# Performance work log

Measured on AMD Instinct MI355X. Metric: run time of the kernel, lower is better.

## Reference

```python
import jax, jax.numpy as jnp
import numpy as np

V, C, H, W = 6, 256, 128, 128


def setup_inputs() -> dict:
    key = jax.random.key(0)
    ks = jax.random.split(key, 6)
    return {
        "q": jax.random.normal(ks[0], (V, C, H, W), dtype=jnp.float32),
        "k": jax.random.normal(ks[1], (V, C, H, W), dtype=jnp.float32),
        "v": jax.random.normal(ks[2], (V, C, H, W), dtype=jnp.float32),
        "Wq": jax.random.normal(ks[3], (C, C), dtype=jnp.float32) * (1.0 / np.sqrt(C)),
        "Wk": jax.random.normal(ks[4], (C, C), dtype=jnp.float32) * (1.0 / np.sqrt(C)),
        "Wv": jax.random.normal(ks[5], (C, C), dtype=jnp.float32) * (1.0 / np.sqrt(C)),
    }


def reference(q, k, v, Wq, Wk, Wv):
    # 1x1 conv (no bias) == channel GEMM: [V,C,H,W] x [O,C] -> [V,O,H,W]
    qp = jnp.einsum("vchw,oc->vohw", q, Wq)
    kp = jnp.einsum("vchw,oc->vohw", k, Wk)
    vp = jnp.einsum("vchw,oc->vohw", v, Wv)
    # elementwise q*k, sum over channels (dim=1, keepdim) -> [V,1,H,W]
    att = jnp.sum(qp * kp, axis=1, keepdims=True)
    # softmax over views (dim=0)
    att = jax.nn.softmax(att, axis=0)
    # weight values and sum over views (dim=0, keepdim) -> [1,C,H,W]
    out = jnp.sum(att * vp, axis=0, keepdims=True)
    return out
```

## Files before the change

kernel.cpp:

```cpp
#include <hip/hip_runtime.h>
#include <math.h>

#define HW 16384
#define C_DIM 256
#define V_DIM 6
#define PT 64
#define BK 32
#define KROW 40

typedef short bf16x8 __attribute__((ext_vector_type(8)));
typedef float f32x4 __attribute__((ext_vector_type(4)));

__device__ __forceinline__ void split2(float x, unsigned short& h,
                                       unsigned short& l) {
    unsigned u = __float_as_uint(x);
    h = (unsigned short)(u >> 16);
    float xl = x - __uint_as_float(u & 0xFFFF0000u);
    l = (unsigned short)(__float_as_uint(xl) >> 16);
}

__global__ void compute_M_kernel(const float* __restrict__ Wq,
                                 const float* __restrict__ Wk,
                                 unsigned short* __restrict__ Mh,
                                 unsigned short* __restrict__ Ml) {
    const int i = blockIdx.x;
    const int j = threadIdx.x;
    float a0 = 0.f, a1 = 0.f, a2 = 0.f, a3 = 0.f;
    #pragma unroll 4
    for (int o = 0; o < C_DIM; o += 4) {
        a0 = fmaf(Wq[(o + 0) * C_DIM + i], Wk[(o + 0) * C_DIM + j], a0);
        a1 = fmaf(Wq[(o + 1) * C_DIM + i], Wk[(o + 1) * C_DIM + j], a1);
        a2 = fmaf(Wq[(o + 2) * C_DIM + i], Wk[(o + 2) * C_DIM + j], a2);
        a3 = fmaf(Wq[(o + 3) * C_DIM + i], Wk[(o + 3) * C_DIM + j], a3);
    }
    float acc = (a0 + a1) + (a2 + a3);
    unsigned short h, l;
    split2(acc, h, l);
    Mh[i * C_DIM + j] = h;
    Ml[i * C_DIM + j] = l;
}

__global__ __launch_bounds__(512, 3) void score_kernel(
        const float* __restrict__ q, const float* __restrict__ k,
        const unsigned short* __restrict__ Mh,
        const unsigned short* __restrict__ Ml,
        float* __restrict__ score) {
    const int tid  = threadIdx.x;
    const int lane = tid & 63;
    const int w    = tid >> 6;
    const int pt   = blockIdx.x & 255;
    const int v    = blockIdx.x >> 8;
    const int gp0  = pt * PT;
    const int l15  = lane & 15;
    const int l4   = lane >> 4;

    __shared__ __align__(16) unsigned short Kh_s[2][PT * KROW];
    __shared__ __align__(16) unsigned short Kl_s[2][PT * KROW];
    __shared__ float s_red[8][PT];

    const float* kv = k + (size_t)v * C_DIM * HW + gp0;
    const float* qv = q + (size_t)v * C_DIM * HW + gp0;
    const int ibase = w * 32;

    f32x4 acc[2][4];
    #pragma unroll
    for (int a = 0; a < 2; ++a)
        #pragma unroll
        for (int b = 0; b < 4; ++b)
            acc[a][b] = (f32x4){0.f, 0.f, 0.f, 0.f};

    float kx[3][4];
    bf16x8 Ah[2][2], Al[2][2];
    float qx[32];

    {
        const float* kp = kv + (size_t)(w * 4) * HW + lane;
        float x[4];
        #pragma unroll
        for (int e = 0; e < 4; ++e) x[e] = kp[(size_t)e * HW];
        unsigned short h[4], l[4];
        #pragma unroll
        for (int e = 0; e < 4; ++e) split2(x[e], h[e], l[e]);
        uint2 H, L;
        H.x = (unsigned)h[0] | ((unsigned)h[1] << 16);
        H.y = (unsigned)h[2] | ((unsigned)h[3] << 16);
        L.x = (unsigned)l[0] | ((unsigned)l[1] << 16);
        L.y = (unsigned)l[2] | ((unsigned)l[3] << 16);
        *(uint2*)&Kh_s[0][lane * KROW + w * 4] = H;
        *(uint2*)&Kl_s[0][lane * KROW + w * 4] = L;

        const float* kp1 = kv + (size_t)(1 * BK + w * 4) * HW + lane;
        #pragma unroll
        for (int e = 0; e < 4; ++e) kx[1][e] = kp1[(size_t)e * HW];
        const float* kp2 = kv + (size_t)(2 * BK + w * 4) * HW + lane;
        #pragma unroll
        for (int e = 0; e < 4; ++e) kx[2][e] = kp2[(size_t)e * HW];

        #pragma unroll
        for (int it = 0; it < 2; ++it) {
            int row = ibase + it * 16 + l15;
            Ah[0][it] = *(const bf16x8*)(Mh + (size_t)row * C_DIM + l4 * 8);
            Al[0][it] = *(const bf16x8*)(Ml + (size_t)row * C_DIM + l4 * 8);
        }
    }
    __syncthreads();

    #pragma unroll
    for (int ks = 0; ks < 8; ++ks) {
        const int cur = ks & 1;

        if (ks < 7) {
            #pragma unroll
            for (int it = 0; it < 2; ++it) {
                int row = ibase + it * 16 + l15;
                Ah[cur ^ 1][it] = *(const bf16x8*)(Mh + (size_t)row * C_DIM +
                                                   (ks + 1) * BK + l4 * 8);
                Al[cur ^ 1][it] = *(const bf16x8*)(Ml + (size_t)row * C_DIM +
                                                   (ks + 1) * BK + l4 * 8);
            }
        }
        if (ks < 5) {
            const float* kp = kv + (size_t)((ks + 3) * BK + w * 4) * HW + lane;
            #pragma unroll
            for (int e = 0; e < 4; ++e) kx[ks % 3][e] = kp[(size_t)e * HW];
        }
        if (ks == 7) {
            #pragma unroll
            for (int jt = 0; jt < 4; ++jt)
                #pragma unroll
                for (int it = 0; it < 2; ++it) {
                    int irow = ibase + it * 16 + l4 * 4;
                    const float* qp = qv + (size_t)irow * HW + jt * 16 + l15;
                    #pragma unroll
                    for (int r = 0; r < 4; ++r)
                        qx[jt * 8 + it * 4 + r] = qp[(size_t)r * HW];
                }
        }

        bf16x8 Bh[4];
        #pragma unroll
        for (int jt = 0; jt < 4; ++jt) {
            int bp = jt * 16 + l15;
            Bh[jt] = *(const bf16x8*)&Kh_s[cur][bp * KROW + l4 * 8];
        }
        #pragma unroll
        for (int it = 0; it < 2; ++it)
            #pragma unroll
            for (int jt = 0; jt < 4; ++jt)
                acc[it][jt] = __builtin_amdgcn_mfma_f32_16x16x32_bf16(
                                  Ah[cur][it], Bh[jt], acc[it][jt], 0, 0, 0);
        #pragma unroll
        for (int it = 0; it < 2; ++it)
            #pragma unroll
            for (int jt = 0; jt < 4; ++jt)
                acc[it][jt] = __builtin_amdgcn_mfma_f32_16x16x32_bf16(
                                  Al[cur][it], Bh[jt], acc[it][jt], 0, 0, 0);
        bf16x8 Bl[4];
        #pragma unroll
        for (int jt = 0; jt < 4; ++jt) {
            int bp = jt * 16 + l15;
            Bl[jt] = *(const bf16x8*)&Kl_s[cur][bp * KROW + l4 * 8];
        }
        #pragma unroll
        for (int it = 0; it < 2; ++it)
            #pragma unroll
            for (int jt = 0; jt < 4; ++jt)
                acc[it][jt] = __builtin_amdgcn_mfma_f32_16x16x32_bf16(
                                  Ah[cur][it], Bl[jt], acc[it][jt], 0, 0, 0);

        if (ks < 7) {
            unsigned short h[4], l[4];
            #pragma unroll
            for (int e = 0; e < 4; ++e) split2(kx[(ks + 1) % 3][e], h[e], l[e]);
            uint2 H, L;
            H.x = (unsigned)h[0] | ((unsigned)h[1] << 16);
            H.y = (unsigned)h[2] | ((unsigned)h[3] << 16);
            L.x = (unsigned)l[0] | ((unsigned)l[1] << 16);
            L.y = (unsigned)l[2] | ((unsigned)l[3] << 16);
            *(uint2*)&Kh_s[cur ^ 1][lane * KROW + w * 4] = H;
            *(uint2*)&Kl_s[cur ^ 1][lane * KROW + w * 4] = L;
            __syncthreads();
        }
    }

    float sp[4];
    #pragma unroll
    for (int jt = 0; jt < 4; ++jt) sp[jt] = 0.f;
    #pragma unroll
    for (int jt = 0; jt < 4; ++jt) {
        #pragma unroll
        for (int it = 0; it < 2; ++it)
            #pragma unroll
            for (int r = 0; r < 4; ++r)
                sp[jt] = fmaf(qx[jt * 8 + it * 4 + r], acc[it][jt][r], sp[jt]);
        sp[jt] += __shfl_xor(sp[jt], 16, 64);
        sp[jt] += __shfl_xor(sp[jt], 32, 64);
    }
    if (lane < 16) {
        #pragma unroll
        for (int jt = 0; jt < 4; ++jt)
            s_red[w][jt * 16 + lane] = sp[jt];
    }
    __syncthreads();
    if (tid < PT) {
        float s = 0.f;
        #pragma unroll
        for (int ww = 0; ww < 8; ++ww) s += s_red[ww][tid];
        score[v * HW + gp0 + tid] = s;
    }
}

__global__ void wsplit_kernel(const float* __restrict__ Wv,
                              unsigned short* __restrict__ Wvh,
                              unsigned short* __restrict__ Wvl) {
    const int i = blockIdx.x;
    const int j = threadIdx.x;
    unsigned short h, l;
    split2(Wv[i * C_DIM + j], h, l);
    Wvh[i * C_DIM + j] = h;
    Wvl[i * C_DIM + j] = l;
}

__global__ __launch_bounds__(512, 2) void out_gemm_kernel(
        const float* __restrict__ vin,
        const unsigned short* __restrict__ Wvh,
        const unsigned short* __restrict__ Wvl,
        const float* __restrict__ score,
        float* __restrict__ out) {
    const int tid  = threadIdx.x;
    const int lane = tid & 63;
    const int w    = tid >> 6;
    const int gp0  = blockIdx.x * PT;
    const int l15  = lane & 15;
    const int l4   = lane >> 4;
    const int jg   = w;

    __shared__ __align__(16) unsigned short Xh_s[2][PT * KROW];
    __shared__ __align__(16) unsigned short Xl_s[2][PT * KROW];

    float wr[V_DIM];
    {
        float s[V_DIM];
        float mx = -1e30f;
        #pragma unroll
        for (int vv = 0; vv < V_DIM; ++vv) {
            s[vv] = score[vv * HW + gp0 + lane];
            mx = fmaxf(mx, s[vv]);
        }
        float sum = 0.f;
        #pragma unroll
        for (int vv = 0; vv < V_DIM; ++vv) {
            s[vv] = __expf(s[vv] - mx);
            sum += s[vv];
        }
        float inv = 1.0f / sum;
        #pragma unroll
        for (int vv = 0; vv < V_DIM; ++vv) wr[vv] = s[vv] * inv;
    }

    const float* vbase = vin + gp0 + lane;
    const int obase = w * 32;

    f32x4 acc[2][4];
    #pragma unroll
    for (int a = 0; a < 2; ++a)
        #pragma unroll
        for (int b = 0; b < 4; ++b)
            acc[a][b] = (f32x4){0.f, 0.f, 0.f, 0.f};

    float vx[2][4][V_DIM];
    bf16x8 Ah[2][2], Al[2][2];

    {
        float x0[4][V_DIM];
        #pragma unroll
        for (int vv = 0; vv < V_DIM; ++vv)
            #pragma unroll
            for (int e = 0; e < 4; ++e)
                x0[e][vv] = vbase[(size_t)(vv * C_DIM + jg * 4 + e) * HW];
        unsigned short h[4], l[4];
        #pragma unroll
        for (int e = 0; e < 4; ++e) {
            float s = 0.f;
            #pragma unroll
            for (int vv = 0; vv < V_DIM; ++vv) s = fmaf(wr[vv], x0[e][vv], s);
            split2(s, h[e], l[e]);
        }
        uint2 H, L;
        H.x = (unsigned)h[0] | ((unsigned)h[1] << 16);
        H.y = (unsigned)h[2] | ((unsigned)h[3] << 16);
        L.x = (unsigned)l[0] | ((unsigned)l[1] << 16);
        L.y = (unsigned)l[2] | ((unsigned)l[3] << 16);
        *(uint2*)&Xh_s[0][lane * KROW + jg * 4] = H;
        *(uint2*)&Xl_s[0][lane * KROW + jg * 4] = L;

        #pragma unroll
        for (int vv = 0; vv < V_DIM; ++vv)
            #pragma unroll
            for (int e = 0; e < 4; ++e)
                vx[1][e][vv] = vbase[(size_t)(vv * C_DIM + BK + jg * 4 + e) * HW];

        #pragma unroll
        for (int it = 0; it < 2; ++it) {
            int row = obase + it * 16 + l15;
            Ah[0][it] = *(const bf16x8*)(Wvh + (size_t)row * C_DIM + l4 * 8);
            Al[0][it] = *(const bf16x8*)(Wvl + (size_t)row * C_DIM + l4 * 8);
        }
    }
    __syncthreads();

    #pragma unroll
    for (int ks = 0; ks < 8; ++ks) {
        const int cur = ks & 1;

        if (ks < 7) {
            #pragma unroll
            for (int it = 0; it < 2; ++it) {
                int row = obase + it * 16 + l15;
                Ah[cur ^ 1][it] = *(const bf16x8*)(Wvh + (size_t)row * C_DIM +
                                                   (ks + 1) * BK + l4 * 8);
                Al[cur ^ 1][it] = *(const bf16x8*)(Wvl + (size_t)row * C_DIM +
                                                   (ks + 1) * BK + l4 * 8);
            }
        }
        if (ks < 6) {
            #pragma unroll
            for (int vv = 0; vv < V_DIM; ++vv)
                #pragma unroll
                for (int e = 0; e < 4; ++e)
                    vx[cur][e][vv] = vbase[(size_t)(vv * C_DIM + (ks + 2) * BK +
                                                    jg * 4 + e) * HW];
        }

        bf16x8 Bh[4], Bl[4];
        #pragma unroll
        for (int jt = 0; jt < 4; ++jt) {
            int bp = jt * 16 + l15;
            Bh[jt] = *(const bf16x8*)&Xh_s[cur][bp * KROW + l4 * 8];
            Bl[jt] = *(const bf16x8*)&Xl_s[cur][bp * KROW + l4 * 8];
        }
        #pragma unroll
        for (int it = 0; it < 2; ++it)
            #pragma unroll
            for (int jt = 0; jt < 4; ++jt)
                acc[it][jt] = __builtin_amdgcn_mfma_f32_16x16x32_bf16(
                                  Ah[cur][it], Bh[jt], acc[it][jt], 0, 0, 0);
        #pragma unroll
        for (int it = 0; it < 2; ++it)
            #pragma unroll
            for (int jt = 0; jt < 4; ++jt)
                acc[it][jt] = __builtin_amdgcn_mfma_f32_16x16x32_bf16(
                                  Ah[cur][it], Bl[jt], acc[it][jt], 0, 0, 0);
        #pragma unroll
        for (int it = 0; it < 2; ++it)
            #pragma unroll
            for (int jt = 0; jt < 4; ++jt)
                acc[it][jt] = __builtin_amdgcn_mfma_f32_16x16x32_bf16(
                                  Al[cur][it], Bh[jt], acc[it][jt], 0, 0, 0);

        if (ks < 7) {
            unsigned short h[4], l[4];
            #pragma unroll
            for (int e = 0; e < 4; ++e) {
                float s = 0.f;
                #pragma unroll
                for (int vv = 0; vv < V_DIM; ++vv)
                    s = fmaf(wr[vv], vx[cur ^ 1][e][vv], s);
                split2(s, h[e], l[e]);
            }
            uint2 H, L;
            H.x = (unsigned)h[0] | ((unsigned)h[1] << 16);
            H.y = (unsigned)h[2] | ((unsigned)h[3] << 16);
            L.x = (unsigned)l[0] | ((unsigned)l[1] << 16);
            L.y = (unsigned)l[2] | ((unsigned)l[3] << 16);
            *(uint2*)&Xh_s[cur ^ 1][lane * KROW + jg * 4] = H;
            *(uint2*)&Xl_s[cur ^ 1][lane * KROW + jg * 4] = L;
        }
        __syncthreads();
    }

    #pragma unroll
    for (int it = 0; it < 2; ++it)
        #pragma unroll
        for (int jt = 0; jt < 4; ++jt)
            #pragma unroll
            for (int r = 0; r < 4; ++r) {
                int o = obase + it * 16 + l4 * 4 + r;
                out[(size_t)o * HW + gp0 + jt * 16 + l15] = acc[it][jt][r];
            }
}

extern "C" void kernel_launch(void* const* d_in, const int* in_sizes, int n_in,
                              void* d_out, int out_size, void* d_ws, size_t ws_size,
                              hipStream_t stream) {
    const float* q  = (const float*)d_in[0];
    const float* k  = (const float*)d_in[1];
    const float* v  = (const float*)d_in[2];
    const float* Wq = (const float*)d_in[3];
    const float* Wk = (const float*)d_in[4];
    const float* Wv = (const float*)d_in[5];
    float* out = (float*)d_out;

    unsigned short* Mh = (unsigned short*)d_ws;
    unsigned short* Ml = Mh + C_DIM * C_DIM;
    float* score = (float*)(Ml + C_DIM * C_DIM);

    compute_M_kernel<<<C_DIM, C_DIM, 0, stream>>>(Wq, Wk, Mh, Ml);
    score_kernel<<<V_DIM * 256, 512, 0, stream>>>(q, k, Mh, Ml, score);
    wsplit_kernel<<<C_DIM, C_DIM, 0, stream>>>(Wv, Mh, Ml);
    out_gemm_kernel<<<HW / PT, 512, 0, stream>>>(v, Mh, Ml, score, out);
}
```

Baseline: 121.4 us.

## Stage full K tile in LDS upfront in score kernel, drop per-step double buffering

The score kernel now loads all eight K slabs for its 64-pixel tile at the start, splits them into bf16 hi/lo and stores them in LDS before a single barrier. The main MFMA loop then runs without the per-step global loads, splits and __syncthreads. Q values are loaded directly in the epilogue instead of being prefetched into 32 registers, and the reduction buffer reuses the K LDS space. Launch bounds rise to 4 blocks per CU to try to raise occupancy, at the cost of a larger LDS footprint (about 80KB per block), which may itself limit how many blocks fit, and less overlap of global loads with compute inside a block.

```diff
diff --git a/kernel.cpp b/kernel.cpp
--- a/kernel.cpp
+++ b/kernel.cpp
@@ -7,6 +7,7 @@
 #define PT 64
 #define BK 32
 #define KROW 40
+#define KT (PT * KROW)
 
 typedef short bf16x8 __attribute__((ext_vector_type(8)));
 typedef float f32x4 __attribute__((ext_vector_type(4)));
@@ -40,7 +41,7 @@
     Ml[i * C_DIM + j] = l;
 }
 
-__global__ __launch_bounds__(512, 3) void score_kernel(
+__global__ __launch_bounds__(512, 4) void score_kernel(
         const float* __restrict__ q, const float* __restrict__ k,
         const unsigned short* __restrict__ Mh,
         const unsigned short* __restrict__ Ml,
@@ -54,14 +55,37 @@
     const int l15  = lane & 15;
     const int l4   = lane >> 4;
 
-    __shared__ __align__(16) unsigned short Kh_s[2][PT * KROW];
-    __shared__ __align__(16) unsigned short Kl_s[2][PT * KROW];
-    __shared__ float s_red[8][PT];
+    __shared__ __align__(16) unsigned short Kh_s[8 * KT];
+    __shared__ __align__(16) unsigned short Kl_s[8 * KT];
 
     const float* kv = k + (size_t)v * C_DIM * HW + gp0;
     const float* qv = q + (size_t)v * C_DIM * HW + gp0;
     const int ibase = w * 32;
 
+    {
+        float kx[8][4];
+        #pragma unroll
+        for (int t = 0; t < 8; ++t) {
+            const float* kp = kv + (size_t)(t * BK + w * 4) * HW + lane;
+            #pragma unroll
+            for (int e = 0; e < 4; ++e) kx[t][e] = kp[(size_t)e * HW];
+        }
+        #pragma unroll
+        for (int t = 0; t < 8; ++t) {
+            unsigned short h[4], l[4];
+            #pragma unroll
+            for (int e = 0; e < 4; ++e) split2(kx[t][e], h[e], l[e]);
+            uint2 H, L;
+            H.x = (unsigned)h[0] | ((unsigned)h[1] << 16);
+            H.y = (unsigned)h[2] | ((unsigned)h[3] << 16);
+            L.x = (unsigned)l[0] | ((unsigned)l[1] << 16);
+            L.y = (unsigned)l[2] | ((unsigned)l[3] << 16);
+            *(uint2*)&Kh_s[t * KT + lane * KROW + w * 4] = H;
+            *(uint2*)&Kl_s[t * KT + lane * KROW + w * 4] = L;
+        }
+    }
+    __syncthreads();
+
     f32x4 acc[2][4];
     #pragma unroll
     for (int a = 0; a < 2; ++a)
@@ -69,41 +93,13 @@
         for (int b = 0; b < 4; ++b)
             acc[a][b] = (f32x4){0.f, 0.f, 0.f, 0.f};
 
-    float kx[3][4];
     bf16x8 Ah[2][2], Al[2][2];
-    float qx[32];
-
-    {
-        const float* kp = kv + (size_t)(w * 4) * HW + lane;
-        float x[4];
-        #pragma unroll
-        for (int e = 0; e < 4; ++e) x[e] = kp[(size_t)e * HW];
-        unsigned short h[4], l[4];
-        #pragma unroll
-        for (int e = 0; e < 4; ++e) split2(x[e], h[e], l[e]);
-        uint2 H, L;
-        H.x = (unsigned)h[0] | ((unsigned)h[1] << 16);
-        H.y = (unsigned)h[2] | ((unsigned)h[3] << 16);
-        L.x = (unsigned)l[0] | ((unsigned)l[1] << 16);
-        L.y = (unsigned)l[2] | ((unsigned)l[3] << 16);
-        *(uint2*)&Kh_s[0][lane * KROW + w * 4] = H;
-        *(uint2*)&Kl_s[0][lane * KROW + w * 4] = L;
-
-        const float* kp1 = kv + (size_t)(1 * BK + w * 4) * HW + lane;
-        #pragma unroll
-        for (int e = 0; e < 4; ++e) kx[1][e] = kp1[(size_t)e * HW];
-        const float* kp2 = kv + (size_t)(2 * BK + w * 4) * HW + lane;
-        #pragma unroll
-        for (int e = 0; e < 4; ++e) kx[2][e] = kp2[(size_t)e * HW];
-
-        #pragma unroll
-        for (int it = 0; it < 2; ++it) {
-            int row = ibase + it * 16 + l15;
-            Ah[0][it] = *(const bf16x8*)(Mh + (size_t)row * C_DIM + l4 * 8);
-            Al[0][it] = *(const bf16x8*)(Ml + (size_t)row * C_DIM + l4 * 8);
-        }
-    }
-    __syncthreads();
+    #pragma unroll
+    for (int it = 0; it < 2; ++it) {
+        int row = ibase + it * 16 + l15;
+        Ah[0][it] = *(const bf16x8*)(Mh + (size_t)row * C_DIM + l4 * 8);
+        Al[0][it] = *(const bf16x8*)(Ml + (size_t)row * C_DIM + l4 * 8);
+    }
 
     #pragma unroll
     for (int ks = 0; ks < 8; ++ks) {
@@ -119,29 +115,12 @@
                                                    (ks + 1) * BK + l4 * 8);
             }
         }
-        if (ks < 5) {
-            const float* kp = kv + (size_t)((ks + 3) * BK + w * 4) * HW + lane;
-            #pragma unroll
-            for (int e = 0; e < 4; ++e) kx[ks % 3][e] = kp[(size_t)e * HW];
-        }
-        if (ks == 7) {
-            #pragma unroll
-            for (int jt = 0; jt < 4; ++jt)
-                #pragma unroll
-                for (int it = 0; it < 2; ++it) {
-                    int irow = ibase + it * 16 + l4 * 4;
-                    const float* qp = qv + (size_t)irow * HW + jt * 16 + l15;
-                    #pragma unroll
-                    for (int r = 0; r < 4; ++r)
-                        qx[jt * 8 + it * 4 + r] = qp[(size_t)r * HW];
-                }
-        }
 
         bf16x8 Bh[4];
         #pragma unroll
         for (int jt = 0; jt < 4; ++jt) {
             int bp = jt * 16 + l15;
-            Bh[jt] = *(const bf16x8*)&Kh_s[cur][bp * KROW + l4 * 8];
+            Bh[jt] = *(const bf16x8*)&Kh_s[ks * KT + bp * KROW + l4 * 8];
         }
         #pragma unroll
         for (int it = 0; it < 2; ++it)
@@ -159,7 +138,7 @@
         #pragma unroll
         for (int jt = 0; jt < 4; ++jt) {
             int bp = jt * 16 + l15;
-            Bl[jt] = *(const bf16x8*)&Kl_s[cur][bp * KROW + l4 * 8];
+            Bl[jt] = *(const bf16x8*)&Kl_s[ks * KT + bp * KROW + l4 * 8];
         }
         #pragma unroll
         for (int it = 0; it < 2; ++it)
@@ -167,20 +146,6 @@
             for (int jt = 0; jt < 4; ++jt)
                 acc[it][jt] = __builtin_amdgcn_mfma_f32_16x16x32_bf16(
                                   Ah[cur][it], Bl[jt], acc[it][jt], 0, 0, 0);
-
-        if (ks < 7) {
-            unsigned short h[4], l[4];
-            #pragma unroll
-            for (int e = 0; e < 4; ++e) split2(kx[(ks + 1) % 3][e], h[e], l[e]);
-            uint2 H, L;
-            H.x = (unsigned)h[0] | ((unsigned)h[1] << 16);
-            H.y = (unsigned)h[2] | ((unsigned)h[3] << 16);
-            L.x = (unsigned)l[0] | ((unsigned)l[1] << 16);
-            L.y = (unsigned)l[2] | ((unsigned)l[3] << 16);
-            *(uint2*)&Kh_s[cur ^ 1][lane * KROW + w * 4] = H;
-            *(uint2*)&Kl_s[cur ^ 1][lane * KROW + w * 4] = L;
-            __syncthreads();
-        }
     }
 
     float sp[4];
@@ -189,23 +154,29 @@
     #pragma unroll
     for (int jt = 0; jt < 4; ++jt) {
         #pragma unroll
-        for (int it = 0; it < 2; ++it)
+        for (int it = 0; it < 2; ++it) {
+            int irow = ibase + it * 16 + l4 * 4;
+            const float* qp = qv + (size_t)irow * HW + jt * 16 + l15;
             #pragma unroll
             for (int r = 0; r < 4; ++r)
-                sp[jt] = fmaf(qx[jt * 8 + it * 4 + r], acc[it][jt][r], sp[jt]);
+                sp[jt] = fmaf(qp[(size_t)r * HW], acc[it][jt][r], sp[jt]);
+        }
         sp[jt] += __shfl_xor(sp[jt], 16, 64);
         sp[jt] += __shfl_xor(sp[jt], 32, 64);
     }
+
+    __syncthreads();
+    float* s_red = (float*)Kh_s;
     if (lane < 16) {
         #pragma unroll
         for (int jt = 0; jt < 4; ++jt)
-            s_red[w][jt * 16 + lane] = sp[jt];
+            s_red[w * PT + jt * 16 + lane] = sp[jt];
     }
     __syncthreads();
     if (tid < PT) {
         float s = 0.f;
         #pragma unroll
-        for (int ww = 0; ww < 8; ++ww) s += s_red[ww][tid];
+        for (int ww = 0; ww < 8; ++ww) s += s_red[ww * PT + tid];
         score[v * HW + gp0 + tid] = s;
     }
 }
@@ -235,8 +206,8 @@
     const int l4   = lane >> 4;
     const int jg   = w;
 
-    __shared__ __align__(16) unsigned short Xh_s[2][PT * KROW];
-    __shared__ __align__(16) unsigned short Xl_s[2][PT * KROW];
+    __shared__ __align__(16) unsigned short Xh_s[2][KT];
+    __shared__ __align__(16) unsigned short Xl_s[2][KT];
 
     float wr[V_DIM];
     {
```

Measured after the change: 121.9 us. Within noise of the previous version (+0.4%).

## Make score kernel loop over all views per block with cross-view prefetch

Applied to the files above, without the earlier changes.

The score kernel now launches one block per 64-pixel tile (256 blocks) and loops over the six views inside each block, instead of one block per (view, tile). The K-tile register prefetch runs continuously across view boundaries, with two-deep register buffering replacing three-deep, so the pipeline is not refilled for each view. Q loads are spread over the first four k-steps. Launch bounds drop to 2 waves per SIMD. With only 256 blocks on a chip with 256 CUs, each CU gets a single block, so latency hiding now depends on overlap within the block rather than on several resident blocks per CU.

```diff
diff --git a/kernel.cpp b/kernel.cpp
--- a/kernel.cpp
+++ b/kernel.cpp
@@ -7,6 +7,7 @@
 #define PT 64
 #define BK 32
 #define KROW 40
+#define KT (PT * KROW)
 
 typedef short bf16x8 __attribute__((ext_vector_type(8)));
 typedef float f32x4 __attribute__((ext_vector_type(4)));
@@ -40,7 +41,7 @@
     Ml[i * C_DIM + j] = l;
 }
 
-__global__ __launch_bounds__(512, 3) void score_kernel(
+__global__ __launch_bounds__(512, 2) void score_kernel(
         const float* __restrict__ q, const float* __restrict__ k,
         const unsigned short* __restrict__ Mh,
         const unsigned short* __restrict__ Ml,
@@ -48,18 +49,14 @@
     const int tid  = threadIdx.x;
     const int lane = tid & 63;
     const int w    = tid >> 6;
-    const int pt   = blockIdx.x & 255;
-    const int v    = blockIdx.x >> 8;
-    const int gp0  = pt * PT;
+    const int gp0  = blockIdx.x * PT;
     const int l15  = lane & 15;
     const int l4   = lane >> 4;
 
-    __shared__ __align__(16) unsigned short Kh_s[2][PT * KROW];
-    __shared__ __align__(16) unsigned short Kl_s[2][PT * KROW];
+    __shared__ __align__(16) unsigned short Kh_s[2][KT];
+    __shared__ __align__(16) unsigned short Kl_s[2][KT];
     __shared__ float s_red[8][PT];
 
-    const float* kv = k + (size_t)v * C_DIM * HW + gp0;
-    const float* qv = q + (size_t)v * C_DIM * HW + gp0;
     const int ibase = w * 32;
 
     f32x4 acc[2][4];
@@ -69,12 +66,12 @@
         for (int b = 0; b < 4; ++b)
             acc[a][b] = (f32x4){0.f, 0.f, 0.f, 0.f};
 
-    float kx[3][4];
     bf16x8 Ah[2][2], Al[2][2];
+    float kreg[2][4];
     float qx[32];
 
     {
-        const float* kp = kv + (size_t)(w * 4) * HW + lane;
+        const float* kp = k + gp0 + (size_t)(w * 4) * HW + lane;
         float x[4];
         #pragma unroll
         for (int e = 0; e < 4; ++e) x[e] = kp[(size_t)e * HW];
@@ -89,12 +86,9 @@
         *(uint2*)&Kh_s[0][lane * KROW + w * 4] = H;
         *(uint2*)&Kl_s[0][lane * KROW + w * 4] = L;
 
-        const float* kp1 = kv + (size_t)(1 * BK + w * 4) * HW + lane;
-        #pragma unroll
-        for (int e = 0; e < 4; ++e) kx[1][e] = kp1[(size_t)e * HW];
-        const float* kp2 = kv + (size_t)(2 * BK + w * 4) * HW + lane;
-        #pragma unroll
-        for (int e = 0; e < 4; ++e) kx[2][e] = kp2[(size_t)e * HW];
+        const float* kp1 = k + gp0 + (size_t)(BK + w * 4) * HW + lane;
+        #pragma unroll
+        for (int e = 0; e < 4; ++e) kreg[1][e] = kp1[(size_t)e * HW];
 
         #pragma unroll
         for (int it = 0; it < 2; ++it) {
@@ -105,28 +99,28 @@
     }
     __syncthreads();
 
-    #pragma unroll
-    for (int ks = 0; ks < 8; ++ks) {
-        const int cur = ks & 1;
-
-        if (ks < 7) {
-            #pragma unroll
-            for (int it = 0; it < 2; ++it) {
-                int row = ibase + it * 16 + l15;
-                Ah[cur ^ 1][it] = *(const bf16x8*)(Mh + (size_t)row * C_DIM +
-                                                   (ks + 1) * BK + l4 * 8);
-                Al[cur ^ 1][it] = *(const bf16x8*)(Ml + (size_t)row * C_DIM +
-                                                   (ks + 1) * BK + l4 * 8);
-            }
-        }
-        if (ks < 5) {
-            const float* kp = kv + (size_t)((ks + 3) * BK + w * 4) * HW + lane;
-            #pragma unroll
-            for (int e = 0; e < 4; ++e) kx[ks % 3][e] = kp[(size_t)e * HW];
-        }
-        if (ks == 7) {
-            #pragma unroll
-            for (int jt = 0; jt < 4; ++jt)
+    for (int v = 0; v < V_DIM; ++v) {
+        const float* qv = q + (size_t)v * C_DIM * HW + gp0;
+
+        #pragma unroll
+        for (int ks = 0; ks < 8; ++ks) {
+            const int cur = ks & 1;
+            const bool last_t  = (v == V_DIM - 1) && (ks == 7);
+            const bool last_t2 = (v == V_DIM - 1) && (ks >= 6);
+
+            if (!last_t) {
+                const int kb = ((ks + 1) & 7) * BK;
+                #pragma unroll
+                for (int it = 0; it < 2; ++it) {
+                    int row = ibase + it * 16 + l15;
+                    Ah[cur ^ 1][it] = *(const bf16x8*)(Mh + (size_t)row * C_DIM +
+                                                       kb + l4 * 8);
+                    Al[cur ^ 1][it] = *(const bf16x8*)(Ml + (size_t)row * C_DIM +
+                                                       kb + l4 * 8);
+                }
+            }
+            if (ks < 4) {
+                const int jt = ks;
                 #pragma unroll
                 for (int it = 0; it < 2; ++it) {
                     int irow = ibase + it * 16 + l4 * 4;
@@ -135,78 +129,95 @@
                     for (int r = 0; r < 4; ++r)
                         qx[jt * 8 + it * 4 + r] = qp[(size_t)r * HW];
                 }
-        }
-
-        bf16x8 Bh[4];
-        #pragma unroll
-        for (int jt = 0; jt < 4; ++jt) {
-            int bp = jt * 16 + l15;
-            Bh[jt] = *(const bf16x8*)&Kh_s[cur][bp * KROW + l4 * 8];
-        }
-        #pragma unroll
-        for (int it = 0; it < 2; ++it)
-            #pragma unroll
-            for (int jt = 0; jt < 4; ++jt)
-                acc[it][jt] = __builtin_amdgcn_mfma_f32_16x16x32_bf16(
-                                  Ah[cur][it], Bh[jt], acc[it][jt], 0, 0, 0);
-        #pragma unroll
-        for (int it = 0; it < 2; ++it)
-            #pragma unroll
-            for (int jt = 0; jt < 4; ++jt)
-                acc[it][jt] = __builtin_amdgcn_mfma_f32_16x16x32_bf16(
-                                  Al[cur][it], Bh[jt], acc[it][jt], 0, 0, 0);
-        bf16x8 Bl[4];
-        #pragma unroll
-        for (int jt = 0; jt < 4; ++jt) {
-            int bp = jt * 16 + l15;
-            Bl[jt] = *(const bf16x8*)&Kl_s[cur][bp * KROW + l4 * 8];
-        }
-        #pragma unroll
-        for (int it = 0; it < 2; ++it)
-            #pragma unroll
-            for (int jt = 0; jt < 4; ++jt)
-                acc[it][jt] = __builtin_amdgcn_mfma_f32_16x16x32_bf16(
-                                  Ah[cur][it], Bl[jt], acc[it][jt], 0, 0, 0);
-
-        if (ks < 7) {
-            unsigned short h[4], l[4];
-            #pragma unroll
-            for (int e = 0; e < 4; ++e) split2(kx[(ks + 1) % 3][e], h[e], l[e]);
-            uint2 H, L;
-            H.x = (unsigned)h[0] | ((unsigned)h[1] << 16);
-            H.y = (unsigned)h[2] | ((unsigned)h[3] << 16);
-            L.x = (unsigned)l[0] | ((unsigned)l[1] << 16);
-            L.y = (unsigned)l[2] | ((unsigned)l[3] << 16);
-            *(uint2*)&Kh_s[cur ^ 1][lane * KROW + w * 4] = H;
-            *(uint2*)&Kl_s[cur ^ 1][lane * KROW + w * 4] = L;
+            }
+            if (!last_t2) {
+                const int v2  = (ks >= 6) ? v + 1 : v;
+                const int kb2 = ((ks + 2) & 7) * BK;
+                const float* kp = k + (size_t)v2 * C_DIM * HW + gp0 +
+                                  (size_t)(kb2 + w * 4) * HW + lane;
+                #pragma unroll
+                for (int e = 0; e < 4; ++e) kreg[cur][e] = kp[(size_t)e * HW];
+            }
+
+            bf16x8 Bh[4];
+            #pragma unroll
+            for (int jt = 0; jt < 4; ++jt) {
+                int bp = jt * 16 + l15;
+                Bh[jt] = *(const bf16x8*)&Kh_s[cur][bp * KROW + l4 * 8];
+            }
+            #pragma unroll
+            for (int it = 0; it < 2; ++it)
+                #pragma unroll
+                for (int jt = 0; jt < 4; ++jt)
+                    acc[it][jt] = __builtin_amdgcn_mfma_f32_16x16x32_bf16(
+                                      Ah[cur][it], Bh[jt], acc[it][jt], 0, 0, 0);
+            #pragma unroll
+            for (int it = 0; it < 2; ++it)
+                #pragma unroll
+                for (int jt = 0; jt < 4; ++jt)
+                    acc[it][jt] = __builtin_amdgcn_mfma_f32_16x16x32_bf16(
+                                      Al[cur][it], Bh[jt], acc[it][jt], 0, 0, 0);
+            bf16x8 Bl[4];
+            #pragma unroll
+            for (int jt = 0; jt < 4; ++jt) {
+                int bp = jt * 16 + l15;
+                Bl[jt] = *(const bf16x8*)&Kl_s[cur][bp * KROW + l4 * 8];
+            }
+            #pragma unroll
+            for (int it = 0; it < 2; ++it)
+                #pragma unroll
+                for (int jt = 0; jt < 4; ++jt)
+                    acc[it][jt] = __builtin_amdgcn_mfma_f32_16x16x32_bf16(
+                                      Ah[cur][it], Bl[jt], acc[it][jt], 0, 0, 0);
+
+            if (ks == 7) {
+                float sp[4];
+                #pragma unroll
+                for (int jt = 0; jt < 4; ++jt) sp[jt] = 0.f;
+                #pragma unroll
+                for (int jt = 0; jt < 4; ++jt) {
+                    #pragma unroll
+                    for (int it = 0; it < 2; ++it)
+                        #pragma unroll
+                        for (int r = 0; r < 4; ++r)
+                            sp[jt] = fmaf(qx[jt * 8 + it * 4 + r],
+                                          acc[it][jt][r], sp[jt]);
+                    sp[jt] += __shfl_xor(sp[jt], 16, 64);
+                    sp[jt] += __shfl_xor(sp[jt], 32, 64);
+                }
+                if (lane < 16) {
+                    #pragma unroll
+                    for (int jt = 0; jt < 4; ++jt)
+                        s_red[w][jt * 16 + lane] = sp[jt];
+                }
+                __syncthreads();
+                if (tid < PT) {
+                    float s = 0.f;
+                    #pragma unroll
+                    for (int ww = 0; ww < 8; ++ww) s += s_red[ww][tid];
+                    score[v * HW + gp0 + tid] = s;
+                }
+                #pragma unroll
+                for (int a = 0; a < 2; ++a)
+                    #pragma unroll
+                    for (int b = 0; b < 4; ++b)
+                        acc[a][b] = (f32x4){0.f, 0.f, 0.f, 0.f};
+            }
+
+            if (!last_t) {
+                unsigned short h[4], l[4];
+                #pragma unroll
+                for (int e = 0; e < 4; ++e) split2(kreg[cur ^ 1][e], h[e], l[e]);
+                uint2 H, L;
+                H.x = (unsigned)h[0] | ((unsigned)h[1] << 16);
+                H.y = (unsigned)h[2] | ((unsigned)h[3] << 16);
+                L.x = (unsigned)l[0] | ((unsigned)l[1] << 16);
+                L.y = (unsigned)l[2] | ((unsigned)l[3] << 16);
+                *(uint2*)&Kh_s[cur ^ 1][lane * KROW + w * 4] = H;
+                *(uint2*)&Kl_s[cur ^ 1][lane * KROW + w * 4] = L;
+            }
             __syncthreads();
         }
-    }
-
-    float sp[4];
-    #pragma unroll
-    for (int jt = 0; jt < 4; ++jt) sp[jt] = 0.f;
-    #pragma unroll
-    for (int jt = 0; jt < 4; ++jt) {
-        #pragma unroll
-        for (int it = 0; it < 2; ++it)
-            #pragma unroll
-            for (int r = 0; r < 4; ++r)
-                sp[jt] = fmaf(qx[jt * 8 + it * 4 + r], acc[it][jt][r], sp[jt]);
-        sp[jt] += __shfl_xor(sp[jt], 16, 64);
-        sp[jt] += __shfl_xor(sp[jt], 32, 64);
-    }
-    if (lane < 16) {
-        #pragma unroll
-        for (int jt = 0; jt < 4; ++jt)
-            s_red[w][jt * 16 + lane] = sp[jt];
-    }
-    __syncthreads();
-    if (tid < PT) {
-        float s = 0.f;
-        #pragma unroll
-        for (int ww = 0; ww < 8; ++ww) s += s_red[ww][tid];
-        score[v * HW + gp0 + tid] = s;
     }
 }
 
@@ -235,8 +246,8 @@
     const int l4   = lane >> 4;
     const int jg   = w;
 
-    __shared__ __align__(16) unsigned short Xh_s[2][PT * KROW];
-    __shared__ __align__(16) unsigned short Xl_s[2][PT * KROW];
+    __shared__ __align__(16) unsigned short Xh_s[2][KT];
+    __shared__ __align__(16) unsigned short Xl_s[2][KT];
 
     float wr[V_DIM];
     {
@@ -406,7 +417,7 @@
     float* score = (float*)(Ml + C_DIM * C_DIM);
 
     compute_M_kernel<<<C_DIM, C_DIM, 0, stream>>>(Wq, Wk, Mh, Ml);
-    score_kernel<<<V_DIM * 256, 512, 0, stream>>>(q, k, Mh, Ml, score);
+    score_kernel<<<HW / PT, 512, 0, stream>>>(q, k, Mh, Ml, score);
     wsplit_kernel<<<C_DIM, C_DIM, 0, stream>>>(Wv, Mh, Ml);
     out_gemm_kernel<<<HW / PT, 512, 0, stream>>>(v, Mh, Ml, score, out);
 }
```

Measured after the change: 107.2 us, median of 3. 11.7% less time.
